# Performance work log

Hardware: AMD Instinct MI355X
Metric: run time of the kernel (lower is better)

The kernel has to match this reference:

```python
import jax, jax.numpy as jnp
import numpy as np

EPS = 1e-8  # torch F.cosine_similarity clamps norms to eps=1e-8

def _normalize(x):
    n = jnp.linalg.norm(x, axis=-1, keepdims=True)
    return x / jnp.maximum(n, EPS)

def _masked_mean(v, mask):
    m = mask.astype(v.dtype)
    return jnp.sum(v * m, axis=-1) / jnp.sum(m, axis=-1)

def setup_inputs() -> dict:
    key = jax.random.key(0)
    k1, k2 = jax.random.split(key)
    B, L1, L2, D = 128, 512, 512, 512
    x1 = jax.random.normal(k1, (B, L1, D), dtype=jnp.float32)
    x2 = jax.random.normal(k2, (B, L2, D), dtype=jnp.float32)
    mask1 = jnp.ones((B, L1), dtype=jnp.int32)
    mask2 = jnp.ones((B, L2), dtype=jnp.int32)
    return {"x1": x1, "mask1": mask1, "x2": x2, "mask2": mask2}

def reference(x1, mask1, x2, mask2):
    # normalized token embeddings
    n1 = _normalize(x1)  # (B, L1, D)
    n2 = _normalize(x2)  # (B, L2, D)
    # masked pairwise cosine similarity (B, L1, L2)
    sim = jnp.einsum('bld,bmd->blm', n1, n2)
    neg_inf = jnp.array(-jnp.inf, dtype=sim.dtype)
    sim = jnp.where(mask1[:, :, None].astype(bool), sim, neg_inf)
    sim = jnp.where(mask2[:, None, :].astype(bool), sim, neg_inf)
    # dual argmax (indices are constants w.r.t. grads, matching torch.no_grad)
    idx1 = jnp.argmax(sim, axis=-1)  # (B, L1): best x2 token per x1 token
    idx2 = jnp.argmax(sim, axis=-2)  # (B, L2): best x1 token per x2 token
    # gather matched partners and recompute per-token cosine sim
    g2 = jnp.take_along_axis(n2, idx1[:, :, None], axis=1)  # (B, L1, D)
    g1 = jnp.take_along_axis(n1, idx2[:, :, None], axis=1)  # (B, L2, D)
    sim1 = jnp.sum(n1 * g2, axis=-1)  # (B, L1)
    sim2 = jnp.sum(g1 * n2, axis=-1)  # (B, L2)
    s1 = _masked_mean(sim1, mask1)
    s2 = _masked_mean(sim2, mask2)
    return (s1 + s2) / 2  # (B,)
```

## Files before the change

kernel.cpp:

```cpp
#include <hip/hip_runtime.h>
#include <hip/hip_bf16.h>

#define NB 128
#define LL 512
#define DD 512

typedef __attribute__((ext_vector_type(4))) float  f32x4;
typedef __attribute__((ext_vector_type(8))) short  s16x8;

#define AS1 __attribute__((address_space(1)))
#define AS3 __attribute__((address_space(3)))

__device__ __forceinline__ short f2bf(float f) {
    __hip_bfloat16 h = __float2bfloat16(f);
    return *reinterpret_cast<short*>(&h);
}

__device__ __forceinline__ unsigned fmap(float f) {
    unsigned u = __float_as_uint(f);
    return (u & 0x80000000u) ? ~u : (u | 0x80000000u);
}
__device__ __forceinline__ float funmap(unsigned u) {
    unsigned b = (u & 0x80000000u) ? (u ^ 0x80000000u) : ~u;
    return __uint_as_float(b);
}

__device__ __forceinline__ void gl16(const void* g, void* l) {
    __builtin_amdgcn_global_load_lds((const AS1 unsigned int*)g,
                                     (AS3 unsigned int*)l, 16, 0, 0);
}

__global__ __launch_bounds__(256) void init_kernel(unsigned* __restrict__ p, int n) {
    int i = blockIdx.x * 256 + threadIdx.x;
    if (i < n) p[i] = 0u;
}

__device__ __forceinline__ void stage32(
        const float* __restrict__ Ab, const float* __restrict__ Bb,
        int k0, char* lds, int w, int lane) {
    #pragma unroll
    for (int p = 0; p < 4; ++p) {
        int base = p * 4096 + w * 1024;
        int L    = base + lane * 16;
        int row  = L >> 7;
        int slot = ((L >> 4) & 7) ^ (row & 7);
        const float* ga = Ab + (size_t)row * DD + k0 + slot * 4;
        gl16(ga, lds + base);
        const float* gb = Bb + (size_t)row * DD + k0 + slot * 4;
        gl16(gb, lds + 16384 + base);
    }
}

__global__ __launch_bounds__(256, 2) void simgemm_fused(
        const float* __restrict__ x1, const float* __restrict__ x2,
        const int* __restrict__ mask1, const int* __restrict__ mask2,
        unsigned* __restrict__ rowmax_u, unsigned* __restrict__ colmax_u) {
    __shared__ __align__(16) char lds[33792];
    float* invA_lds = reinterpret_cast<float*>(lds + 32768);
    float* invB_lds = reinterpret_cast<float*>(lds + 33280);

    int bid = blockIdx.x;
    int lid = (bid & 7) * 256 + (bid >> 3);
    int b   = lid >> 4;
    int tr  = (lid >> 2) & 3;
    int tc  = lid & 3;

    int tid  = threadIdx.x;
    int lane = tid & 63;
    int w    = tid >> 6;
    int wr = w >> 1, wc = w & 1;
    int l15 = lane & 15, lhi = lane >> 4;

    const float* Ab = x1 + ((size_t)b * LL + tr * 128) * DD;
    const float* Bb = x2 + ((size_t)b * LL + tc * 128) * DD;

    float ssa[4] = {0.f, 0.f, 0.f, 0.f};
    float ssb[4] = {0.f, 0.f, 0.f, 0.f};

    f32x4 acc[4][4];
    #pragma unroll
    for (int fr = 0; fr < 4; ++fr)
        #pragma unroll
        for (int fc = 0; fc < 4; ++fc) {
            acc[fr][fc].x = 0.f; acc[fr][fc].y = 0.f;
            acc[fr][fc].z = 0.f; acc[fr][fc].w = 0.f;
        }

    stage32(Ab, Bb, 0, lds, w, lane);
    __syncthreads();

    for (int t = 0; t < 16; ++t) {
        const char* As = lds;
        const char* Bs = lds + 16384;

        s16x8 bfr[4];
        #pragma unroll
        for (int fc = 0; fc < 4; ++fc) {
            int crow = wc * 64 + fc * 16 + l15;
            int s0 = (lhi * 2)     ^ (crow & 7);
            int s1 = (lhi * 2 + 1) ^ (crow & 7);
            f32x4 v0 = *reinterpret_cast<const f32x4*>(Bs + crow * 128 + s0 * 16);
            f32x4 v1 = *reinterpret_cast<const f32x4*>(Bs + crow * 128 + s1 * 16);
            if (wr == 0)
                ssb[fc] += v0.x*v0.x + v0.y*v0.y + v0.z*v0.z + v0.w*v0.w
                         + v1.x*v1.x + v1.y*v1.y + v1.z*v1.z + v1.w*v1.w;
            s16x8 o;
            o[0] = f2bf(v0.x); o[1] = f2bf(v0.y); o[2] = f2bf(v0.z); o[3] = f2bf(v0.w);
            o[4] = f2bf(v1.x); o[5] = f2bf(v1.y); o[6] = f2bf(v1.z); o[7] = f2bf(v1.w);
            bfr[fc] = o;
        }
        #pragma unroll
        for (int fr = 0; fr < 4; ++fr) {
            int row = wr * 64 + fr * 16 + l15;
            int s0 = (lhi * 2)     ^ (row & 7);
            int s1 = (lhi * 2 + 1) ^ (row & 7);
            f32x4 v0 = *reinterpret_cast<const f32x4*>(As + row * 128 + s0 * 16);
            f32x4 v1 = *reinterpret_cast<const f32x4*>(As + row * 128 + s1 * 16);
            if (wc == 0)
                ssa[fr] += v0.x*v0.x + v0.y*v0.y + v0.z*v0.z + v0.w*v0.w
                         + v1.x*v1.x + v1.y*v1.y + v1.z*v1.z + v1.w*v1.w;
            s16x8 a;
            a[0] = f2bf(v0.x); a[1] = f2bf(v0.y); a[2] = f2bf(v0.z); a[3] = f2bf(v0.w);
            a[4] = f2bf(v1.x); a[5] = f2bf(v1.y); a[6] = f2bf(v1.z); a[7] = f2bf(v1.w);
            #pragma unroll
            for (int fc = 0; fc < 4; ++fc)
                acc[fr][fc] = __builtin_amdgcn_mfma_f32_16x16x32_bf16(
                    a, bfr[fc], acc[fr][fc], 0, 0, 0);
        }

        __syncthreads();
        if (t < 15) {
            stage32(Ab, Bb, (t + 1) * 32, lds, w, lane);
            __syncthreads();
        }
    }

    #pragma unroll
    for (int i = 0; i < 4; ++i) {
        ssa[i] += __shfl_xor(ssa[i], 16, 64);
        ssa[i] += __shfl_xor(ssa[i], 32, 64);
        ssb[i] += __shfl_xor(ssb[i], 16, 64);
        ssb[i] += __shfl_xor(ssb[i], 32, 64);
    }
    if (wc == 0 && lhi == 0) {
        #pragma unroll
        for (int fr = 0; fr < 4; ++fr)
            invA_lds[wr * 64 + fr * 16 + l15] = 1.0f / fmaxf(sqrtf(ssa[fr]), 1e-8f);
    }
    if (wr == 0 && lhi == 0) {
        #pragma unroll
        for (int fc = 0; fc < 4; ++fc)
            invB_lds[wc * 64 + fc * 16 + l15] = 1.0f / fmaxf(sqrtf(ssb[fc]), 1e-8f);
    }
    __syncthreads();

    float ia[4][4], ib4[4];
    #pragma unroll
    for (int fr = 0; fr < 4; ++fr)
        #pragma unroll
        for (int r = 0; r < 4; ++r)
            ia[fr][r] = invA_lds[wr * 64 + fr * 16 + lhi * 4 + r];
    #pragma unroll
    for (int fc = 0; fc < 4; ++fc)
        ib4[fc] = invB_lds[wc * 64 + fc * 16 + l15];
    #pragma unroll
    for (int fr = 0; fr < 4; ++fr)
        #pragma unroll
        for (int fc = 0; fc < 4; ++fc)
            #pragma unroll
            for (int r = 0; r < 4; ++r)
                acc[fr][fc][r] *= ia[fr][r] * ib4[fc];

    int m2[4];
    #pragma unroll
    for (int fc = 0; fc < 4; ++fc)
        m2[fc] = mask2[b * LL + tc * 128 + wc * 64 + fc * 16 + l15];
    int m1[4][4];
    #pragma unroll
    for (int fr = 0; fr < 4; ++fr)
        #pragma unroll
        for (int r = 0; r < 4; ++r)
            m1[fr][r] = mask1[b * LL + tr * 128 + wr * 64 + fr * 16 + lhi * 4 + r];

    #pragma unroll
    for (int fr = 0; fr < 4; ++fr) {
        #pragma unroll
        for (int r = 0; r < 4; ++r) {
            float v = -INFINITY;
            #pragma unroll
            for (int fc = 0; fc < 4; ++fc)
                if (m2[fc]) v = fmaxf(v, acc[fr][fc][r]);
            v = fmaxf(v, __shfl_xor(v, 1, 64));
            v = fmaxf(v, __shfl_xor(v, 2, 64));
            v = fmaxf(v, __shfl_xor(v, 4, 64));
            v = fmaxf(v, __shfl_xor(v, 8, 64));
            if (l15 == 0)
                atomicMax(&rowmax_u[b * LL + tr * 128 + wr * 64 + fr * 16 + lhi * 4 + r],
                          fmap(v));
        }
    }
    #pragma unroll
    for (int fc = 0; fc < 4; ++fc) {
        float v = -INFINITY;
        #pragma unroll
        for (int fr = 0; fr < 4; ++fr)
            #pragma unroll
            for (int r = 0; r < 4; ++r)
                if (m1[fr][r]) v = fmaxf(v, acc[fr][fc][r]);
        v = fmaxf(v, __shfl_xor(v, 16, 64));
        v = fmaxf(v, __shfl_xor(v, 32, 64));
        if (lhi == 0)
            atomicMax(&colmax_u[b * LL + tc * 128 + wc * 64 + fc * 16 + l15], fmap(v));
    }
}

__global__ __launch_bounds__(64) void finalize_kernel(
        const unsigned* __restrict__ rowmax_u, const unsigned* __restrict__ colmax_u,
        const int* __restrict__ mask1, const int* __restrict__ mask2,
        float* __restrict__ out) {
    int b = blockIdx.x;
    int lane = threadIdx.x;
    float s1 = 0.f, c1 = 0.f, s2 = 0.f, c2 = 0.f;
    for (int i = lane; i < LL; i += 64) {
        if (mask1[b * LL + i]) { s1 += funmap(rowmax_u[b * LL + i]); c1 += 1.f; }
        if (mask2[b * LL + i]) { s2 += funmap(colmax_u[b * LL + i]); c2 += 1.f; }
    }
    #pragma unroll
    for (int off = 32; off >= 1; off >>= 1) {
        s1 += __shfl_xor(s1, off, 64);
        c1 += __shfl_xor(c1, off, 64);
        s2 += __shfl_xor(s2, off, 64);
        c2 += __shfl_xor(c2, off, 64);
    }
    if (lane == 0) out[b] = 0.5f * (s1 / c1 + s2 / c2);
}

extern "C" void kernel_launch(void* const* d_in, const int* in_sizes, int n_in,
                              void* d_out, int out_size, void* d_ws, size_t ws_size,
                              hipStream_t stream) {
    const float* x1    = (const float*)d_in[0];
    const int*   mask1 = (const int*)d_in[1];
    const float* x2    = (const float*)d_in[2];
    const int*   mask2 = (const int*)d_in[3];
    float* out = (float*)d_out;

    unsigned* rowmax_u = (unsigned*)d_ws;
    unsigned* colmax_u = rowmax_u + NB * LL;

    init_kernel<<<(2 * NB * LL + 255) / 256, 256, 0, stream>>>(rowmax_u, 2 * NB * LL);
    simgemm_fused<<<NB * 16, 256, 0, stream>>>(x1, x2, mask1, mask2,
                                               rowmax_u, colmax_u);
    finalize_kernel<<<NB, 64, 0, stream>>>(rowmax_u, colmax_u, mask1, mask2, out);
}
```

Baseline: 116.6 us.

## Load GEMM operands straight from global to registers, dropping LDS staging and barriers

```diff
diff --git a/kernel.cpp b/kernel.cpp
--- a/kernel.cpp
+++ b/kernel.cpp
@@ -8,9 +8,6 @@
 typedef __attribute__((ext_vector_type(4))) float  f32x4;
 typedef __attribute__((ext_vector_type(8))) short  s16x8;
 
-#define AS1 __attribute__((address_space(1)))
-#define AS3 __attribute__((address_space(3)))
-
 __device__ __forceinline__ short f2bf(float f) {
     __hip_bfloat16 h = __float2bfloat16(f);
     return *reinterpret_cast<short*>(&h);
@@ -25,40 +22,15 @@
     return __uint_as_float(b);
 }
 
-__device__ __forceinline__ void gl16(const void* g, void* l) {
-    __builtin_amdgcn_global_load_lds((const AS1 unsigned int*)g,
-                                     (AS3 unsigned int*)l, 16, 0, 0);
-}
-
 __global__ __launch_bounds__(256) void init_kernel(unsigned* __restrict__ p, int n) {
     int i = blockIdx.x * 256 + threadIdx.x;
     if (i < n) p[i] = 0u;
 }
 
-__device__ __forceinline__ void stage32(
-        const float* __restrict__ Ab, const float* __restrict__ Bb,
-        int k0, char* lds, int w, int lane) {
-    #pragma unroll
-    for (int p = 0; p < 4; ++p) {
-        int base = p * 4096 + w * 1024;
-        int L    = base + lane * 16;
-        int row  = L >> 7;
-        int slot = ((L >> 4) & 7) ^ (row & 7);
-        const float* ga = Ab + (size_t)row * DD + k0 + slot * 4;
-        gl16(ga, lds + base);
-        const float* gb = Bb + (size_t)row * DD + k0 + slot * 4;
-        gl16(gb, lds + 16384 + base);
-    }
-}
-
-__global__ __launch_bounds__(256, 2) void simgemm_fused(
+__global__ __launch_bounds__(256, 3) void simdirect(
         const float* __restrict__ x1, const float* __restrict__ x2,
         const int* __restrict__ mask1, const int* __restrict__ mask2,
         unsigned* __restrict__ rowmax_u, unsigned* __restrict__ colmax_u) {
-    __shared__ __align__(16) char lds[33792];
-    float* invA_lds = reinterpret_cast<float*>(lds + 32768);
-    float* invB_lds = reinterpret_cast<float*>(lds + 33280);
-
     int bid = blockIdx.x;
     int lid = (bid & 7) * 256 + (bid >> 3);
     int b   = lid >> 4;
@@ -71,8 +43,8 @@
     int wr = w >> 1, wc = w & 1;
     int l15 = lane & 15, lhi = lane >> 4;
 
-    const float* Ab = x1 + ((size_t)b * LL + tr * 128) * DD;
-    const float* Bb = x2 + ((size_t)b * LL + tc * 128) * DD;
+    const float* Ab = x1 + ((size_t)b * LL + tr * 128 + wr * 64) * DD;
+    const float* Bb = x2 + ((size_t)b * LL + tc * 128 + wc * 64) * DD;
 
     float ssa[4] = {0.f, 0.f, 0.f, 0.f};
     float ssb[4] = {0.f, 0.f, 0.f, 0.f};
@@ -86,53 +58,42 @@
             acc[fr][fc].z = 0.f; acc[fr][fc].w = 0.f;
         }
 
-    stage32(Ab, Bb, 0, lds, w, lane);
-    __syncthreads();
-
-    for (int t = 0; t < 16; ++t) {
-        const char* As = lds;
-        const char* Bs = lds + 16384;
-
-        s16x8 bfr[4];
+    #pragma unroll
+    for (int ks = 0; ks < 16; ++ks) {
+        int kof = ks * 32 + lhi * 8;
+        s16x8 af[4], bf[4];
+        #pragma unroll
+        for (int fr = 0; fr < 4; ++fr) {
+            const float* g = Ab + (size_t)(fr * 16 + l15) * DD + kof;
+            f32x4 v0 = *reinterpret_cast<const f32x4*>(g);
+            f32x4 v1 = *reinterpret_cast<const f32x4*>(g + 4);
+            ssa[fr] += v0.x*v0.x + v0.y*v0.y + v0.z*v0.z + v0.w*v0.w
+                     + v1.x*v1.x + v1.y*v1.y + v1.z*v1.z + v1.w*v1.w;
+            s16x8 a;
+            a[0] = f2bf(v0.x); a[1] = f2bf(v0.y); a[2] = f2bf(v0.z); a[3] = f2bf(v0.w);
+            a[4] = f2bf(v1.x); a[5] = f2bf(v1.y); a[6] = f2bf(v1.z); a[7] = f2bf(v1.w);
+            af[fr] = a;
+        }
         #pragma unroll
         for (int fc = 0; fc < 4; ++fc) {
-            int crow = wc * 64 + fc * 16 + l15;
-            int s0 = (lhi * 2)     ^ (crow & 7);
-            int s1 = (lhi * 2 + 1) ^ (crow & 7);
-            f32x4 v0 = *reinterpret_cast<const f32x4*>(Bs + crow * 128 + s0 * 16);
-            f32x4 v1 = *reinterpret_cast<const f32x4*>(Bs + crow * 128 + s1 * 16);
-            if (wr == 0)
-                ssb[fc] += v0.x*v0.x + v0.y*v0.y + v0.z*v0.z + v0.w*v0.w
-                         + v1.x*v1.x + v1.y*v1.y + v1.z*v1.z + v1.w*v1.w;
+            const float* g = Bb + (size_t)(fc * 16 + l15) * DD + kof;
+            f32x4 v0 = *reinterpret_cast<const f32x4*>(g);
+            f32x4 v1 = *reinterpret_cast<const f32x4*>(g + 4);
+            ssb[fc] += v0.x*v0.x + v0.y*v0.y + v0.z*v0.z + v0.w*v0.w
+                     + v1.x*v1.x + v1.y*v1.y + v1.z*v1.z + v1.w*v1.w;
             s16x8 o;
             o[0] = f2bf(v0.x); o[1] = f2bf(v0.y); o[2] = f2bf(v0.z); o[3] = f2bf(v0.w);
             o[4] = f2bf(v1.x); o[5] = f2bf(v1.y); o[6] = f2bf(v1.z); o[7] = f2bf(v1.w);
-            bfr[fc] = o;
-        }
-        #pragma unroll
-        for (int fr = 0; fr < 4; ++fr) {
-            int row = wr * 64 + fr * 16 + l15;
-            int s0 = (lhi * 2)     ^ (row & 7);
-            int s1 = (lhi * 2 + 1) ^ (row & 7);
-            f32x4 v0 = *reinterpret_cast<const f32x4*>(As + row * 128 + s0 * 16);
-            f32x4 v1 = *reinterpret_cast<const f32x4*>(As + row * 128 + s1 * 16);
-            if (wc == 0)
-                ssa[fr] += v0.x*v0.x + v0.y*v0.y + v0.z*v0.z + v0.w*v0.w
-                         + v1.x*v1.x + v1.y*v1.y + v1.z*v1.z + v1.w*v1.w;
-            s16x8 a;
-            a[0] = f2bf(v0.x); a[1] = f2bf(v0.y); a[2] = f2bf(v0.z); a[3] = f2bf(v0.w);
-            a[4] = f2bf(v1.x); a[5] = f2bf(v1.y); a[6] = f2bf(v1.z); a[7] = f2bf(v1.w);
+            bf[fc] = o;
+        }
+        __builtin_amdgcn_s_setprio(1);
+        #pragma unroll
+        for (int fr = 0; fr < 4; ++fr)
             #pragma unroll
             for (int fc = 0; fc < 4; ++fc)
                 acc[fr][fc] = __builtin_amdgcn_mfma_f32_16x16x32_bf16(
-                    a, bfr[fc], acc[fr][fc], 0, 0, 0);
-        }
-
-        __syncthreads();
-        if (t < 15) {
-            stage32(Ab, Bb, (t + 1) * 32, lds, w, lane);
-            __syncthreads();
-        }
+                    af[fr], bf[fc], acc[fr][fc], 0, 0, 0);
+        __builtin_amdgcn_s_setprio(0);
     }
 
     #pragma unroll
@@ -142,27 +103,16 @@
         ssb[i] += __shfl_xor(ssb[i], 16, 64);
         ssb[i] += __shfl_xor(ssb[i], 32, 64);
     }
-    if (wc == 0 && lhi == 0) {
-        #pragma unroll
-        for (int fr = 0; fr < 4; ++fr)
-            invA_lds[wr * 64 + fr * 16 + l15] = 1.0f / fmaxf(sqrtf(ssa[fr]), 1e-8f);
-    }
-    if (wr == 0 && lhi == 0) {
-        #pragma unroll
-        for (int fc = 0; fc < 4; ++fc)
-            invB_lds[wc * 64 + fc * 16 + l15] = 1.0f / fmaxf(sqrtf(ssb[fc]), 1e-8f);
-    }
-    __syncthreads();
-
     float ia[4][4], ib4[4];
     #pragma unroll
     for (int fr = 0; fr < 4; ++fr)
         #pragma unroll
         for (int r = 0; r < 4; ++r)
-            ia[fr][r] = invA_lds[wr * 64 + fr * 16 + lhi * 4 + r];
+            ia[fr][r] = 1.0f / fmaxf(sqrtf(__shfl(ssa[fr], lhi * 4 + r, 16)), 1e-8f);
     #pragma unroll
     for (int fc = 0; fc < 4; ++fc)
-        ib4[fc] = invB_lds[wc * 64 + fc * 16 + l15];
+        ib4[fc] = 1.0f / fmaxf(sqrtf(ssb[fc]), 1e-8f);
+
     #pragma unroll
     for (int fr = 0; fr < 4; ++fr)
         #pragma unroll
@@ -248,7 +198,7 @@
     unsigned* colmax_u = rowmax_u + NB * LL;
 
     init_kernel<<<(2 * NB * LL + 255) / 256, 256, 0, stream>>>(rowmax_u, 2 * NB * LL);
-    simgemm_fused<<<NB * 16, 256, 0, stream>>>(x1, x2, mask1, mask2,
-                                               rowmax_u, colmax_u);
+    simdirect<<<NB * 16, 256, 0, stream>>>(x1, x2, mask1, mask2,
+                                           rowmax_u, colmax_u);
     finalize_kernel<<<NB, 64, 0, stream>>>(rowmax_u, colmax_u, mask1, mask2, out);
 }
```

After: 282.7 us. +142.4%, slower.
